# Performance work log

Hardware: AMD Instinct MI355X
Metric: run time of the kernel (lower is better)

The kernel has to match this reference:

```python
import jax, jax.numpy as jnp
import numpy as np

N, E, F_IN, HID, HEADS, NG, NC = 50000, 800000, 128, 64, 4, 64, 10
NEG_SLOPE = 0.2


def gat_conv(h_in, src, dst, W, att_src, att_dst, bias, heads, out_ch, concat, num_nodes):
    # h_in: [N, Fin]; W: [Fin, heads*out_ch]; att_*: [heads, out_ch]; bias: [heads*out_ch] or [out_ch]
    h = (h_in @ W).reshape(num_nodes, heads, out_ch)            # [N,H,C]
    a_src = jnp.sum(h * att_src, axis=-1)                        # [N,H]
    a_dst = jnp.sum(h * att_dst, axis=-1)                        # [N,H]
    alpha = jax.nn.leaky_relu(a_src[src] + a_dst[dst], NEG_SLOPE)  # [Etot,H]
    # softmax over incoming edges per destination node
    amax = jax.ops.segment_max(alpha, dst, num_segments=num_nodes)
    amax = jnp.where(jnp.isfinite(amax), amax, 0.0)
    ex = jnp.exp(alpha - amax[dst])
    denom = jax.ops.segment_sum(ex, dst, num_segments=num_nodes)
    w = ex / (denom[dst] + 1e-16)                                # [Etot,H]
    msg = h[src] * w[:, :, None]                                 # [Etot,H,C]
    out = jax.ops.segment_sum(msg, dst, num_segments=num_nodes)  # [N,H,C]
    out = out.reshape(num_nodes, heads * out_ch) if concat else out.mean(axis=1)
    return out + bias


def setup_inputs() -> dict:
    key = jax.random.key(0)
    ks = jax.random.split(key, 20)
    s = lambda k, shp, f: (jax.random.normal(k, shp, jnp.float32) * f)
    return {
        "x": jax.random.normal(ks[0], (N, F_IN), jnp.float32),
        "edge_index": jax.random.randint(ks[1], (2, E), 0, N, jnp.int32),
        "batch": jax.random.randint(ks[2], (N,), 0, NG, jnp.int32),
        "W_proj": s(ks[3], (F_IN, HID), 0.05), "b_proj": jnp.zeros((HID,), jnp.float32),
        "W1": s(ks[4], (HID, HEADS * HID), 0.05),
        "att_src1": s(ks[5], (HEADS, HID), 0.1), "att_dst1": s(ks[6], (HEADS, HID), 0.1),
        "b1": jnp.zeros((HEADS * HID,), jnp.float32),
        "W2": s(ks[7], (HEADS * HID, HID), 0.05),
        "att_src2": s(ks[8], (1, HID), 0.1), "att_dst2": s(ks[9], (1, HID), 0.1),
        "b2": jnp.zeros((HID,), jnp.float32),
        "W_fc1": s(ks[10], (HID, HID // 2), 0.05), "b_fc1": jnp.zeros((HID // 2,), jnp.float32),
        "W_fc2": s(ks[11], (HID // 2, NC), 0.05), "b_fc2": jnp.zeros((NC,), jnp.float32),
    }


def reference(x, edge_index, batch, W_proj, b_proj, W1, att_src1, att_dst1, b1,
              W2, att_src2, att_dst2, b2, W_fc1, b_fc1, W_fc2, b_fc2):
    n = x.shape[0]
    loops = jnp.arange(n, dtype=edge_index.dtype)  # PyG GATConv add_self_loops=True
    src = jnp.concatenate([edge_index[0], loops])
    dst = jnp.concatenate([edge_index[1], loops])
    h = jax.nn.relu(x @ W_proj + b_proj)                                  # feature_proj + relu
    h = gat_conv(h, src, dst, W1, att_src1, att_dst1, b1, HEADS, HID, True, n)
    h = jax.nn.leaky_relu(h, NEG_SLOPE)                                    # dropout = identity (eval)
    h = gat_conv(h, src, dst, W2, att_src2, att_dst2, b2, 1, HID, False, n)
    h = jax.nn.leaky_relu(h, NEG_SLOPE)
    cnt = jax.ops.segment_sum(jnp.ones((n,), h.dtype), batch, num_segments=NG)
    gmean = jax.ops.segment_sum(h, batch, num_segments=NG) / jnp.maximum(cnt, 1.0)[:, None]
    gmax = jax.ops.segment_max(h, batch, num_segments=NG)
    gmax = jnp.where(jnp.isfinite(gmax), gmax, 0.0)
    g = gmean + gmax
    g = jax.nn.relu(g @ W_fc1 + b_fc1)
    return jax.nn.log_softmax(g @ W_fc2 + b_fc2, axis=1)
```

## Files before the change

kernel.cpp:

```cpp
#include <hip/hip_runtime.h>
#include <math.h>

#define NN 50000
#define EE 800000
#define ET 850000
#define FIN 128
#define HD 64
#define NH 4
#define NGR 64
#define NCL 10
#define NEG 0.2f

typedef unsigned short u16;
typedef unsigned char u8;
typedef unsigned int u32;
typedef __attribute__((ext_vector_type(8))) short short8;
typedef __attribute__((ext_vector_type(4))) float f32x4;

__device__ __forceinline__ float lrelu(float x){ return x > 0.f ? x : NEG * x; }

__device__ __forceinline__ float wsum(float v){
#pragma unroll
  for (int o = 32; o > 0; o >>= 1) v += __shfl_xor(v, o, 64);
  return v;
}
__device__ __forceinline__ float wmax(float v){
#pragma unroll
  for (int o = 32; o > 0; o >>= 1) v = fmaxf(v, __shfl_xor(v, o, 64));
  return v;
}
__device__ __forceinline__ int esrc(const int* ei, int e){ return e < EE ? ei[e] : e - EE; }
__device__ __forceinline__ int edst(const int* ei, int e){ return e < EE ? ei[EE + e] : e - EE; }

__device__ __forceinline__ unsigned f2key(float f){
  unsigned u = __float_as_uint(f);
  return (u & 0x80000000u) ? ~u : (u | 0x80000000u);
}
__device__ __forceinline__ float key2f(unsigned k){
  return (k & 0x80000000u) ? __uint_as_float(k & 0x7fffffffu) : __uint_as_float(~k);
}

__device__ __forceinline__ u16 f2b(float f){
  u32 u = __float_as_uint(f);
  u32 r = (u + 0x7FFFu + ((u >> 16) & 1u)) >> 16;
  return (u16)r;
}
__device__ __forceinline__ float b2f(u16 b){ return __uint_as_float(((u32)b) << 16); }
__device__ __forceinline__ u32 pkbf16(float lo, float hi){
  u32 r;
  asm("v_cvt_pk_bf16_f32 %0, %1, %2" : "=v"(r) : "v"(lo), "v"(hi));
  return r;
}
__device__ __forceinline__ u8 f2fp8(float f){
  return (u8)__builtin_amdgcn_cvt_pk_fp8_f32(f, 0.f, 0, false);
}
__device__ __forceinline__ int rl(int v, int idx){ return __builtin_amdgcn_readlane(v, idx); }
__device__ __forceinline__ float rlf(float v, int idx){
  return __uint_as_float((u32)__builtin_amdgcn_readlane((int)__float_as_uint(v), idx));
}

__global__ __launch_bounds__(256) void k_phf(const int* __restrict__ ei, int* __restrict__ cnt,
            int* __restrict__ rank,
            const float* __restrict__ x, const float* __restrict__ Wp, const float* __restrict__ bp,
            const float* __restrict__ W1, const float* __restrict__ as1, const float* __restrict__ ad1,
            u8* __restrict__ h1f8, float* __restrict__ a_s, float* __restrict__ a_d, int gb){
  __shared__ u16 As[64*(FIN+8)];
  __shared__ u16 h0s[64*(HD+8)];
  int b = blockIdx.x;
  if (b >= gb){
    int base = (b - gb)*1024;
#pragma unroll
    for (int k = 0; k < 4; ++k){
      int e = base + k*256 + threadIdx.x;
      if (e < ET){
        int d = edst(ei, e);
        rank[e] = atomicAdd(&cnt[d], 1);
      }
    }
    return;
  }
  constexpr int LDK1 = FIN + 8;
  constexpr int LDH  = HD + 8;
  int t = threadIdx.x, w = t >> 6, l = t & 63;
  int l16 = l & 15, kg = l >> 4;

  short8 bfp[4];
#pragma unroll
  for (int kt = 0; kt < 4; ++kt){
    short8 v;
#pragma unroll
    for (int j = 0; j < 8; ++j) v[j] = (short)f2b(Wp[(size_t)(kt*32 + kg*8 + j)*HD + w*16 + l16]);
    bfp[kt] = v;
  }
  short8 bf1[2*4];
#pragma unroll
  for (int kt = 0; kt < 2; ++kt)
#pragma unroll
    for (int nt = 0; nt < 4; ++nt){
      short8 v;
#pragma unroll
      for (int j = 0; j < 8; ++j) v[j] = (short)f2b(W1[(size_t)(kt*32 + kg*8 + j)*256 + w*64 + nt*16 + l16]);
      bf1[kt*4 + nt] = v;
    }
  float bv = bp[w*16 + l16];
  float asv[4], adv[4];
#pragma unroll
  for (int nt = 0; nt < 4; ++nt){
    asv[nt] = as1[w*64 + nt*16 + l16];
    adv[nt] = ad1[w*64 + nt*16 + l16];
  }

  for (int ch = 0; ch < 2; ++ch){
    int nb = (b*2 + ch)*64;
    if (nb >= NN) break;
    __syncthreads();
    for (int u = t; u < 64*16; u += 256){
      int r = u >> 4, c = u & 15;
      int n = nb + r;
      uint4 v = make_uint4(0u,0u,0u,0u);
      if (n < NN){
        float4 f0 = *(const float4*)&x[(size_t)n*FIN + c*8];
        float4 f1 = *(const float4*)&x[(size_t)n*FIN + c*8 + 4];
        v = make_uint4(pkbf16(f0.x,f0.y), pkbf16(f0.z,f0.w), pkbf16(f1.x,f1.y), pkbf16(f1.z,f1.w));
      }
      *(uint4*)&As[r*LDK1 + c*8] = v;
    }
    __syncthreads();
#pragma unroll
    for (int rt = 0; rt < 4; ++rt){
      short8 afp[4];
#pragma unroll
      for (int kt = 0; kt < 4; ++kt)
        afp[kt] = *(const short8*)&As[(rt*16 + l16)*LDK1 + kt*32 + kg*8];
      f32x4 acc = (f32x4){0.f,0.f,0.f,0.f};
#pragma unroll
      for (int kt = 0; kt < 4; ++kt)
        acc = __builtin_amdgcn_mfma_f32_16x16x32_bf16(afp[kt], bfp[kt], acc, 0, 0, 0);
#pragma unroll
      for (int r4 = 0; r4 < 4; ++r4)
        h0s[(rt*16 + kg*4 + r4)*LDH + w*16 + l16] = f2b(fmaxf(acc[r4] + bv, 0.f));
    }
    __syncthreads();
#pragma unroll
    for (int rt = 0; rt < 4; ++rt){
      short8 af[2];
#pragma unroll
      for (int kt = 0; kt < 2; ++kt)
        af[kt] = *(const short8*)&h0s[(rt*16 + l16)*LDH + kt*32 + kg*8];
      f32x4 acc[4];
#pragma unroll
      for (int nt = 0; nt < 4; ++nt){
        acc[nt] = (f32x4){0.f,0.f,0.f,0.f};
#pragma unroll
        for (int kt = 0; kt < 2; ++kt)
          acc[nt] = __builtin_amdgcn_mfma_f32_16x16x32_bf16(af[kt], bf1[kt*4 + nt], acc[nt], 0, 0, 0);
      }
      int rbase = nb + rt*16 + kg*4;
#pragma unroll
      for (int nt = 0; nt < 4; ++nt)
#pragma unroll
        for (int r4 = 0; r4 < 4; ++r4){
          int n = rbase + r4;
          if (n < NN) h1f8[(size_t)n*256 + w*64 + nt*16 + l16] = f2fp8(acc[nt][r4]);
        }
#pragma unroll
      for (int r4 = 0; r4 < 4; ++r4){
        float ps = 0.f, pd = 0.f;
#pragma unroll
        for (int nt = 0; nt < 4; ++nt){
          ps = fmaf(acc[nt][r4], asv[nt], ps);
          pd = fmaf(acc[nt][r4], adv[nt], pd);
        }
#pragma unroll
        for (int o = 1; o < 16; o <<= 1){
          ps += __shfl_xor(ps, o, 64);
          pd += __shfl_xor(pd, o, 64);
        }
        int n = rbase + r4;
        if (l16 == 0 && n < NN){ a_s[n*NH + w] = ps; a_d[n*NH + w] = pd; }
      }
    }
  }
}

template<int K, int NOUT, int CPW>
__device__ __forceinline__ void gemm_body2(int bid, u16* As, float* sred,
            const u16* __restrict__ A, const float* __restrict__ Bf,
            const float* __restrict__ att_s, const float* __restrict__ att_d,
            u16* __restrict__ C, float* __restrict__ a_s, float* __restrict__ a_d){
  constexpr int KT = K/32;
  constexpr int NT = CPW/16;
  constexpr int LDK = K + 8;
  int t = threadIdx.x, w = t >> 6, l = t & 63;
  int c0 = w*CPW;
  int l16 = l & 15, kg = l >> 4;

  short8 bf[KT*NT];
#pragma unroll
  for (int kt = 0; kt < KT; ++kt)
#pragma unroll
    for (int nt = 0; nt < NT; ++nt){
      int kbase = kt*32 + kg*8;
      int col = c0 + nt*16 + l16;
      short8 v;
#pragma unroll
      for (int j = 0; j < 8; ++j) v[j] = (short)f2b(Bf[(size_t)(kbase + j)*NOUT + col]);
      bf[kt*NT + nt] = v;
    }
  float asv = att_s[c0 + l16], adv = att_d[c0 + l16];

  for (int ch = 0; ch < 2; ++ch){
    int nb = (bid*2 + ch)*64;
    if (nb >= NN) break;
    __syncthreads();
    constexpr int UPR = K/8;
    for (int u = t; u < 64*UPR; u += 256){
      int r = u / UPR, c = u % UPR;
      int n = nb + r;
      uint4 v = make_uint4(0u,0u,0u,0u);
      if (n < NN) v = *(const uint4*)&A[(size_t)n*K + c*8];
      *(uint4*)&As[r*LDK + c*8] = v;
    }
    __syncthreads();
#pragma unroll
    for (int rt = 0; rt < 4; ++rt){
      short8 af[KT];
#pragma unroll
      for (int kt = 0; kt < KT; ++kt)
        af[kt] = *(const short8*)&As[(rt*16 + l16)*LDK + kt*32 + kg*8];
      f32x4 acc = (f32x4){0.f,0.f,0.f,0.f};
#pragma unroll
      for (int kt = 0; kt < KT; ++kt)
        acc = __builtin_amdgcn_mfma_f32_16x16x32_bf16(af[kt], bf[kt], acc, 0, 0, 0);
      int rbase = nb + rt*16 + kg*4;
#pragma unroll
      for (int r4 = 0; r4 < 4; ++r4){
        int n = rbase + r4;
        if (n < NN) C[(size_t)n*NOUT + c0 + l16] = f2b(acc[r4]);
      }
#pragma unroll
      for (int r4 = 0; r4 < 4; ++r4){
        float ps = acc[r4]*asv;
        float pd = acc[r4]*adv;
#pragma unroll
        for (int o = 1; o < 16; o <<= 1){
          ps += __shfl_xor(ps, o, 64);
          pd += __shfl_xor(pd, o, 64);
        }
        if (l16 == 0){
          int row = rt*16 + kg*4 + r4;
          sred[(w*64 + row)*2]     = ps;
          sred[(w*64 + row)*2 + 1] = pd;
        }
      }
    }
    __syncthreads();
    if (t < 64){
      int n = nb + t;
      if (n < NN){
        float s = sred[t*2] + sred[(64+t)*2] + sred[(128+t)*2] + sred[(192+t)*2];
        float d = sred[t*2+1] + sred[(64+t)*2+1] + sred[(128+t)*2+1] + sred[(192+t)*2+1];
        a_s[n] = s; a_d[n] = d;
      }
    }
  }
}

__global__ void k_bsum(const int* __restrict__ cnt, int* __restrict__ bsums){
  int b = blockIdx.x, t = threadIdx.x;
  int i = b*256 + t;
  int v = (i < NN) ? cnt[i] : 0;
  float s = wsum((float)v);
  __shared__ float ws4[4];
  if ((t & 63) == 0) ws4[t >> 6] = s;
  __syncthreads();
  if (t == 0) bsums[b] = (int)(ws4[0] + ws4[1] + ws4[2] + ws4[3] + 0.5f);
}

__global__ __launch_bounds__(256) void k_off2(const int* __restrict__ cnt, const int* __restrict__ bsums,
                                              int* __restrict__ off){
  int b = blockIdx.x, t = threadIdx.x;
  int i = b*256 + t;
  __shared__ int s[256];
  __shared__ int w4[4];
  int v = (i < NN) ? cnt[i] : 0;
  s[t] = v; __syncthreads();
  for (int d = 1; d < 256; d <<= 1){
    int xv = (t >= d) ? s[t-d] : 0;
    __syncthreads();
    s[t] += xv;
    __syncthreads();
  }
  int pv = (t < b) ? bsums[t] : 0;
  int r = pv;
#pragma unroll
  for (int o2 = 32; o2 > 0; o2 >>= 1) r += __shfl_xor(r, o2, 64);
  if ((t & 63) == 0) w4[t >> 6] = r;
  __syncthreads();
  int pre = w4[0] + w4[1] + w4[2] + w4[3];
  if (i < NN) off[i] = pre + s[t] - v;
  if (i == NN - 1) off[NN] = pre + s[t];
}

__global__ __launch_bounds__(256) void k_scatter(const int* __restrict__ ei, const int* __restrict__ off,
            const int* __restrict__ rank, u16* __restrict__ csrc){
  int base = blockIdx.x*1024;
#pragma unroll
  for (int k = 0; k < 4; ++k){
    int e = base + k*256 + threadIdx.x;
    if (e < ET){
      int d = edst(ei, e);
      int s = esrc(ei, e);
      csrc[off[d] + rank[e]] = (u16)s;
    }
  }
}

__global__ __launch_bounds__(256) void k_feat2(const u16* __restrict__ h1outb, const float* __restrict__ W2,
            const float* __restrict__ as2, const float* __restrict__ ad2,
            u16* __restrict__ h2b, float* __restrict__ a_s, float* __restrict__ a_d){
  __shared__ u16 As[64*(256+8)];
  __shared__ float sred[4*64*2];
  gemm_body2<256, 64, 16>(blockIdx.x, As, sred, h1outb, W2, as2, ad2, h2b, a_s, a_d);
}

__global__ __launch_bounds__(256) void k_gat1(const u8* __restrict__ h1f8, const float* __restrict__ a_s,
                       const float* __restrict__ a_d, const int* __restrict__ off,
                       const u16* __restrict__ csrc, const float* __restrict__ b1,
                       u16* __restrict__ h1outb){
  __shared__ float lw[4][4][68];
  int wv = threadIdx.x >> 6, l = threadIdx.x & 63;
  int n = blockIdx.x*4 + wv;
  if (n >= NN) return;
  int e0 = off[n], e1 = off[n+1], deg = e1 - e0;
  int j16 = l & 15, h = l >> 4;
  float adst = a_d[n*NH + h];
  float acc0 = 0.f, acc1 = 0.f, acc2 = 0.f, acc3 = 0.f;
  const u8* base = h1f8 + 4*l;

#define GAT1_FMA8(wrd, wq) { \
  acc0 = fmaf(__builtin_amdgcn_cvt_f32_fp8((int)(wrd), 0), wq, acc0); \
  acc1 = fmaf(__builtin_amdgcn_cvt_f32_fp8((int)(wrd), 1), wq, acc1); \
  acc2 = fmaf(__builtin_amdgcn_cvt_f32_fp8((int)(wrd), 2), wq, acc2); \
  acc3 = fmaf(__builtin_amdgcn_cvt_f32_fp8((int)(wrd), 3), wq, acc3); }

  if (deg <= 64){
    int sreg[4]; float wreg[4];
#pragma unroll
    for (int c = 0; c < 4; ++c){
      int idx = c*16 + j16;
      int s = (idx < deg) ? (int)csrc[e0 + idx] : 0;
      sreg[c] = s;
      wreg[c] = (idx < deg) ? lrelu(a_s[s*NH + h] + adst) : -3.0e38f;
    }
    float m = fmaxf(fmaxf(wreg[0], wreg[1]), fmaxf(wreg[2], wreg[3]));
#pragma unroll
    for (int o2 = 1; o2 < 16; o2 <<= 1) m = fmaxf(m, __shfl_xor(m, o2, 64));
    float se = 0.f;
#pragma unroll
    for (int c = 0; c < 4; ++c){
      int idx = c*16 + j16;
      float wc = (idx < deg) ? __expf(wreg[c] - m) : 0.f;
      wreg[c] = wc; se += wc;
    }
#pragma unroll
    for (int o2 = 1; o2 < 16; o2 <<= 1) se += __shfl_xor(se, o2, 64);
    float inv = 1.f / (se + 1e-16f);
#pragma unroll
    for (int c = 0; c < 4; ++c) lw[wv][h][c*16 + j16] = wreg[c] * inv;

#pragma unroll
    for (int c = 0; c < 4; ++c){
      int cbase = c*16;
      if (cbase < deg){
        int cnt = deg - cbase; if (cnt > 16) cnt = 16;
        int j2 = 0;
        for (; j2 + 8 <= cnt; j2 += 8){
          float4 wqa = *(const float4*)&lw[wv][h][cbase + j2];
          float4 wqb = *(const float4*)&lw[wv][h][cbase + j2 + 4];
          int s0 = rl(sreg[c], j2),   s1 = rl(sreg[c], j2+1);
          int s2 = rl(sreg[c], j2+2), s3 = rl(sreg[c], j2+3);
          int s4 = rl(sreg[c], j2+4), s5 = rl(sreg[c], j2+5);
          int s6 = rl(sreg[c], j2+6), s7 = rl(sreg[c], j2+7);
          u32 w0 = *(const u32*)(base + (size_t)(u32)s0*256);
          u32 w1 = *(const u32*)(base + (size_t)(u32)s1*256);
          u32 w2 = *(const u32*)(base + (size_t)(u32)s2*256);
          u32 w3 = *(const u32*)(base + (size_t)(u32)s3*256);
          u32 w4 = *(const u32*)(base + (size_t)(u32)s4*256);
          u32 w5 = *(const u32*)(base + (size_t)(u32)s5*256);
          u32 w6 = *(const u32*)(base + (size_t)(u32)s6*256);
          u32 w7 = *(const u32*)(base + (size_t)(u32)s7*256);
          GAT1_FMA8(w0, wqa.x) GAT1_FMA8(w1, wqa.y) GAT1_FMA8(w2, wqa.z) GAT1_FMA8(w3, wqa.w)
          GAT1_FMA8(w4, wqb.x) GAT1_FMA8(w5, wqb.y) GAT1_FMA8(w6, wqb.z) GAT1_FMA8(w7, wqb.w)
        }
        for (; j2 + 4 <= cnt; j2 += 4){
          float4 wq = *(const float4*)&lw[wv][h][cbase + j2];
          int s0 = rl(sreg[c], j2),   s1 = rl(sreg[c], j2+1);
          int s2 = rl(sreg[c], j2+2), s3 = rl(sreg[c], j2+3);
          u32 w0 = *(const u32*)(base + (size_t)(u32)s0*256);
          u32 w1 = *(const u32*)(base + (size_t)(u32)s1*256);
          u32 w2 = *(const u32*)(base + (size_t)(u32)s2*256);
          u32 w3 = *(const u32*)(base + (size_t)(u32)s3*256);
          GAT1_FMA8(w0, wq.x) GAT1_FMA8(w1, wq.y) GAT1_FMA8(w2, wq.z) GAT1_FMA8(w3, wq.w)
        }
        for (; j2 < cnt; ++j2){
          float wqs = lw[wv][h][cbase + j2];
          int s = rl(sreg[c], j2);
          u32 wd = *(const u32*)(base + (size_t)(u32)s*256);
          GAT1_FMA8(wd, wqs)
        }
      }
    }
  } else {
    float m = -3.0e38f;
    for (int i = e0 + j16; i < e1; i += 16){
      int s = csrc[i];
      m = fmaxf(m, lrelu(a_s[s*NH + h] + adst));
    }
#pragma unroll
    for (int o2 = 1; o2 < 16; o2 <<= 1) m = fmaxf(m, __shfl_xor(m, o2, 64));
    float se = 0.f;
    for (int i = e0 + j16; i < e1; i += 16){
      int s = csrc[i];
      se += __expf(lrelu(a_s[s*NH + h] + adst) - m);
    }
#pragma unroll
    for (int o2 = 1; o2 < 16; o2 <<= 1) se += __shfl_xor(se, o2, 64);
    float inv = 1.f / (se + 1e-16f);
    for (int i = e0; i < e1; ++i){
      int s = csrc[i];
      float wq = __expf(lrelu(a_s[s*NH + h] + adst) - m) * inv;
      u32 wd = *(const u32*)(base + (size_t)(u32)s*256);
      GAT1_FMA8(wd, wq)
    }
  }
  float4 bv = *(const float4*)&b1[4*l];
  u32 lo = pkbf16(lrelu(acc0 + bv.x), lrelu(acc1 + bv.y));
  u32 hi = pkbf16(lrelu(acc2 + bv.z), lrelu(acc3 + bv.w));
  *(uint2*)&h1outb[(size_t)n*256 + 4*l] = make_uint2(lo, hi);
}

__global__ __launch_bounds__(256) void k_gat2(const u16* __restrict__ h2b, const float* __restrict__ a_s,
                       const float* __restrict__ a_d, const int* __restrict__ off,
                       const u16* __restrict__ csrc, const float* __restrict__ b2v,
                       float* __restrict__ h2out){
  int wv = threadIdx.x >> 6, l = threadIdx.x & 63;
  int n = blockIdx.x*4 + wv;
  if (n >= NN) return;
  int e0 = off[n], e1 = off[n+1], deg = e1 - e0;
  float adst = a_d[n];
  if (deg <= 64){
    int sA = 0; float alA = -3.0e38f;
    if (l < deg){
      sA = (int)csrc[e0 + l];
      alA = lrelu(a_s[sA] + adst);
    }
    float m = wmax(alA);
    float wA = (l < deg) ? __expf(alA - m) : 0.f;
    float se = wsum(wA);
    wA *= 1.f / (se + 1e-16f);
    float acc = 0.f;
    int idx = 0;
    for (; idx + 8 <= deg; idx += 8){
      int s0 = rl(sA, idx),   s1 = rl(sA, idx+1);
      int s2 = rl(sA, idx+2), s3 = rl(sA, idx+3);
      int s4 = rl(sA, idx+4), s5 = rl(sA, idx+5);
      int s6 = rl(sA, idx+6), s7 = rl(sA, idx+7);
      float w0 = rlf(wA, idx),   w1 = rlf(wA, idx+1);
      float w2 = rlf(wA, idx+2), w3 = rlf(wA, idx+3);
      float w4 = rlf(wA, idx+4), w5 = rlf(wA, idx+5);
      float w6 = rlf(wA, idx+6), w7 = rlf(wA, idx+7);
      float v0 = b2f(h2b[(size_t)(u32)s0*HD + l]);
      float v1 = b2f(h2b[(size_t)(u32)s1*HD + l]);
      float v2 = b2f(h2b[(size_t)(u32)s2*HD + l]);
      float v3 = b2f(h2b[(size_t)(u32)s3*HD + l]);
      float v4 = b2f(h2b[(size_t)(u32)s4*HD + l]);
      float v5 = b2f(h2b[(size_t)(u32)s5*HD + l]);
      float v6 = b2f(h2b[(size_t)(u32)s6*HD + l]);
      float v7 = b2f(h2b[(size_t)(u32)s7*HD + l]);
      acc = fmaf(v0, w0, acc); acc = fmaf(v1, w1, acc);
      acc = fmaf(v2, w2, acc); acc = fmaf(v3, w3, acc);
      acc = fmaf(v4, w4, acc); acc = fmaf(v5, w5, acc);
      acc = fmaf(v6, w6, acc); acc = fmaf(v7, w7, acc);
    }
    for (; idx < deg; ++idx){
      int s = rl(sA, idx);
      float w = rlf(wA, idx);
      acc = fmaf(b2f(h2b[(size_t)(u32)s*HD + l]), w, acc);
    }
    h2out[(size_t)n*HD + l] = lrelu(acc + b2v[l]);
  } else {
    float m = -3.0e38f;
    for (int i = e0 + l; i < e1; i += 64){
      int s = csrc[i];
      m = fmaxf(m, lrelu(a_s[s] + adst));
    }
    m = wmax(m);
    float se = 0.f;
    for (int i = e0 + l; i < e1; i += 64){
      int s = csrc[i];
      se += __expf(lrelu(a_s[s] + adst) - m);
    }
    se = wsum(se);
    float inv = 1.f / (se + 1e-16f);
    float acc = 0.f;
    for (int i = e0; i < e1; ++i){
      int s = csrc[i];
      acc += b2f(h2b[(size_t)s*HD + l]) * __expf(lrelu(a_s[s] + adst) - m);
    }
    h2out[(size_t)n*HD + l] = lrelu(acc*inv + b2v[l]);
  }
}


__global__ void k_pool(const float* __restrict__ h2out, const int* __restrict__ batch,
                       float* __restrict__ gsum, unsigned* __restrict__ gmaxk, int* __restrict__ gcnt){
  __shared__ float ssum[NGR*HD];
  __shared__ unsigned smax[NGR*HD];
  __shared__ int scnt[NGR];
  int t = threadIdx.x;
  for (int i = t; i < NGR*HD; i += 256){ ssum[i] = 0.f; smax[i] = 0u; }
  if (t < NGR) scnt[t] = 0;
  __syncthreads();
  int wv = t >> 6, lane = t & 63;
  for (int n = blockIdx.x*4 + wv; n < NN; n += gridDim.x*4){
    int g = batch[n];
    float v = h2out[(size_t)n*HD + lane];
    atomicAdd(&ssum[g*HD + lane], v);
    atomicMax(&smax[g*HD + lane], f2key(v));
    if (lane == 0) atomicAdd(&scnt[g], 1);
  }
  __syncthreads();
  for (int i = t; i < NGR*HD; i += 256){
    atomicAdd(&gsum[i], ssum[i]);
    atomicMax(&gmaxk[i], smax[i]);
  }
  if (t < NGR) atomicAdd(&gcnt[t], scnt[t]);
}


__global__ void k_final(const float* __restrict__ gsum, const unsigned* __restrict__ gmaxk,
                        const int* __restrict__ gcnt,
                        const float* __restrict__ Wf1, const float* __restrict__ bf1,
                        const float* __restrict__ Wf2, const float* __restrict__ bf2,
                        float* __restrict__ out){
  int g = blockIdx.x, t = threadIdx.x;
  __shared__ float gv[HD];
  __shared__ float f1[32];
  __shared__ float lg[NCL];
  int c = gcnt[g];
  float dn = fmaxf((float)c, 1.f);
  float mean = gsum[g*HD + t] / dn;
  float mx = (c > 0) ? key2f(gmaxk[g*HD + t]) : 0.f;
  gv[t] = mean + mx;
  __syncthreads();
  if (t < 32){
    float a = bf1[t];
#pragma unroll
    for (int k = 0; k < HD; ++k) a += gv[k] * Wf1[k*32 + t];
    f1[t] = a > 0.f ? a : 0.f;
  }
  __syncthreads();
  if (t < NCL){
    float a = bf2[t];
#pragma unroll
    for (int k = 0; k < 32; ++k) a += f1[k] * Wf2[k*NCL + t];
    lg[t] = a;
  }
  __syncthreads();
  if (t < NCL){
    float m = lg[0];
#pragma unroll
    for (int i = 1; i < NCL; ++i) m = fmaxf(m, lg[i]);
    float s = 0.f;
#pragma unroll
    for (int i = 0; i < NCL; ++i) s += expf(lg[i] - m);
    out[g*NCL + t] = lg[t] - m - logf(s);
  }
}

extern "C" void kernel_launch(void* const* d_in, const int* in_sizes, int n_in,
                              void* d_out, int out_size, void* d_ws, size_t ws_size,
                              hipStream_t stream) {
  const float* x   = (const float*)d_in[0];
  const int*   ei  = (const int*)d_in[1];
  const int*   bat = (const int*)d_in[2];
  const float* Wp  = (const float*)d_in[3];
  const float* bp  = (const float*)d_in[4];
  const float* W1  = (const float*)d_in[5];
  const float* as1 = (const float*)d_in[6];
  const float* ad1 = (const float*)d_in[7];
  const float* b1  = (const float*)d_in[8];
  const float* W2  = (const float*)d_in[9];
  const float* as2 = (const float*)d_in[10];
  const float* ad2 = (const float*)d_in[11];
  const float* b2  = (const float*)d_in[12];
  const float* Wf1 = (const float*)d_in[13];
  const float* bf1 = (const float*)d_in[14];
  const float* Wf2 = (const float*)d_in[15];
  const float* bf2 = (const float*)d_in[16];
  float* out = (float*)d_out;

  char* base = (char*)d_ws;
  size_t o = 0;
  auto alloc = [&](size_t elems) -> char* {
    char* p = base + o*4;
    o += (elems + 63) & ~(size_t)63;
    return p;
  };
  u8*    h1f8   = (u8*)alloc(3200000);
  u16*   h1outb = (u16*)alloc(6400000);
  u16*   h2b    = (u16*)alloc(1600000);
  float* h2out  = (float*)alloc(3200000);
  float* a_s1   = (float*)alloc(200000);
  float* a_d1   = (float*)alloc(200000);
  float* a_s2   = (float*)alloc(50000);
  float* a_d2   = (float*)alloc(50000);
  int*   off    = (int*)alloc(50001);
  int*   rank   = (int*)alloc(850000);
  int*   bsums  = (int*)alloc(256);
  u16*   csrc   = (u16*)alloc(425000);
  int*   cnt    = (int*)alloc(50000);
  float* gsum   = (float*)alloc(NGR*HD);
  unsigned* gmaxk = (unsigned*)alloc(NGR*HD);
  int*   gcnt   = (int*)alloc(NGR);

  const int NB  = (NN + 255) / 256;
  const int EB4 = (ET + 1023) / 1024;
  const int GB  = (NN + 127) / 128;
  const int WB  = (NN + 3) / 4;

  hipMemsetAsync(cnt, 0, NN*sizeof(int), stream);
  hipMemsetAsync(gsum, 0, (NGR*HD*2 + 64)*sizeof(int), stream);

  k_phf<<<GB + EB4, 256, 0, stream>>>(ei, cnt, rank, x, Wp, bp, W1, as1, ad1, h1f8, a_s1, a_d1, GB);
  k_bsum<<<NB, 256, 0, stream>>>(cnt, bsums);
  k_off2<<<NB, 256, 0, stream>>>(cnt, bsums, off);
  k_scatter<<<EB4, 256, 0, stream>>>(ei, off, rank, csrc);

  k_gat1<<<WB, 256, 0, stream>>>(h1f8, a_s1, a_d1, off, csrc, b1, h1outb);

  k_feat2<<<GB, 256, 0, stream>>>(h1outb, W2, as2, ad2, h2b, a_s2, a_d2);
  k_gat2<<<WB, 256, 0, stream>>>(h2b, a_s2, a_d2, off, csrc, b2, h2out);

  k_pool<<<256, 256, 0, stream>>>(h2out, bat, gsum, gmaxk, gcnt);

  k_final<<<NGR, 64, 0, stream>>>(gsum, gmaxk, gcnt, Wf1, bf1, Wf2, bf2, out);
}
```

Baseline: 201.3 us.

## Build CSR via two-level bucketed radix partition instead of global atomics

Replaces the per-edge global atomic counting plus rank/scatter pipeline with a two-pass bucket partition. Edges are first grouped into 256-node buckets using per-block LDS histograms and a scan. Each bucket's edges are then finished inside a block of the fused projection kernel, using LDS atomics to produce the offsets and the sorted source list. This is meant to cut global atomic contention and make the scatter writes more local. The cost is extra kernels, more scans and a packed intermediate buffer. It also simplifies gemm_body2's B-fragment load to a single N tile.

```diff
diff --git a/kernel.cpp b/kernel.cpp
--- a/kernel.cpp
+++ b/kernel.cpp
@@ -10,6 +10,8 @@
 #define NGR 64
 #define NCL 10
 #define NEG 0.2f
+#define NBK 196
+#define ECH 831
 
 typedef unsigned short u16;
 typedef unsigned char u8;
@@ -29,6 +31,11 @@
   for (int o = 32; o > 0; o >>= 1) v = fmaxf(v, __shfl_xor(v, o, 64));
   return v;
 }
+__device__ __forceinline__ int wsumi(int v){
+#pragma unroll
+  for (int o = 32; o > 0; o >>= 1) v += __shfl_xor(v, o, 64);
+  return v;
+}
 __device__ __forceinline__ int esrc(const int* ei, int e){ return e < EE ? ei[e] : e - EE; }
 __device__ __forceinline__ int edst(const int* ei, int e){ return e < EE ? ei[EE + e] : e - EE; }
 
@@ -59,29 +66,127 @@
   return __uint_as_float((u32)__builtin_amdgcn_readlane((int)__float_as_uint(v), idx));
 }
 
-__global__ __launch_bounds__(256) void k_phf(const int* __restrict__ ei, int* __restrict__ cnt,
-            int* __restrict__ rank,
+__global__ __launch_bounds__(256) void k_b1hist(const int* __restrict__ ei, int* __restrict__ bcnt){
+  __shared__ int lc[NBK];
+  int t = threadIdx.x, blk = blockIdx.x;
+  for (int i = t; i < NBK; i += 256) lc[i] = 0;
+  __syncthreads();
+#pragma unroll
+  for (int k = 0; k < 4; ++k){
+    int e = blk*1024 + k*256 + t;
+    if (e < ET) atomicAdd(&lc[edst(ei, e) >> 8], 1);
+  }
+  __syncthreads();
+  for (int i = t; i < NBK; i += 256) bcnt[i*ECH + blk] = lc[i];
+}
+
+__global__ __launch_bounds__(256) void k_bscana(const int* __restrict__ bcnt, int* __restrict__ btot){
+  int b = blockIdx.x, t = threadIdx.x;
+  int s = 0;
+  for (int j = t; j < ECH; j += 256) s += bcnt[b*ECH + j];
+  s = wsumi(s);
+  __shared__ int w4[4];
+  if ((t & 63) == 0) w4[t >> 6] = s;
+  __syncthreads();
+  if (t == 0) btot[b] = w4[0] + w4[1] + w4[2] + w4[3];
+}
+
+__global__ __launch_bounds__(256) void k_bscanb(const int* __restrict__ bcnt, const int* __restrict__ btot,
+                                                int* __restrict__ boff, int* __restrict__ bb){
+  int b = blockIdx.x, t = threadIdx.x;
+  int pv = (t < b) ? btot[t] : 0;
+  int r = wsumi(pv);
+  __shared__ int w4[4];
+  if ((t & 63) == 0) w4[t >> 6] = r;
+  __syncthreads();
+  int base = w4[0] + w4[1] + w4[2] + w4[3];
+  if (t == 0) bb[b] = base;
+  __shared__ int s[256];
+  int carry = 0;
+  for (int j0 = 0; j0 < ECH; j0 += 256){
+    int j = j0 + t;
+    int v = (j < ECH) ? bcnt[b*ECH + j] : 0;
+    s[t] = v; __syncthreads();
+    for (int d = 1; d < 256; d <<= 1){
+      int xv = (t >= d) ? s[t-d] : 0;
+      __syncthreads();
+      s[t] += xv;
+      __syncthreads();
+    }
+    int excl = s[t] - v;
+    if (j < ECH) boff[b*ECH + j] = base + carry + excl;
+    int tot = s[255];
+    __syncthreads();
+    carry += tot;
+  }
+}
+
+__global__ __launch_bounds__(256) void k_b1scat(const int* __restrict__ ei, const int* __restrict__ boff,
+                                                u32* __restrict__ packed){
+  __shared__ int lpos[NBK];
+  int t = threadIdx.x, blk = blockIdx.x;
+  for (int i = t; i < NBK; i += 256) lpos[i] = boff[i*ECH + blk];
+  __syncthreads();
+#pragma unroll
+  for (int k = 0; k < 4; ++k){
+    int e = blk*1024 + k*256 + t;
+    if (e < ET){
+      int d = edst(ei, e);
+      int s = esrc(ei, e);
+      int slot = atomicAdd(&lpos[d >> 8], 1);
+      packed[slot] = ((u32)(d & 255) << 16) | (u32)s;
+    }
+  }
+}
+
+__global__ __launch_bounds__(256) void k_phf2(
+            const u32* __restrict__ packed, const int* __restrict__ btot, const int* __restrict__ bb,
+            int* __restrict__ off, u16* __restrict__ csrc,
             const float* __restrict__ x, const float* __restrict__ Wp, const float* __restrict__ bp,
             const float* __restrict__ W1, const float* __restrict__ as1, const float* __restrict__ ad1,
             u8* __restrict__ h1f8, float* __restrict__ a_s, float* __restrict__ a_d, int gb){
   __shared__ u16 As[64*(FIN+8)];
   __shared__ u16 h0s[64*(HD+8)];
-  int b = blockIdx.x;
-  if (b >= gb){
-    int base = (b - gb)*1024;
-#pragma unroll
-    for (int k = 0; k < 4; ++k){
-      int e = base + k*256 + threadIdx.x;
-      if (e < ET){
-        int d = edst(ei, e);
-        rank[e] = atomicAdd(&cnt[d], 1);
-      }
+  __shared__ int hc[256];
+  __shared__ int sc[256];
+  __shared__ int pp[256];
+  int t = threadIdx.x;
+  int bid = blockIdx.x;
+  if (bid >= gb){
+    int b = bid - gb;
+    int e0 = bb[b];
+    int cntb = btot[b];
+    hc[t] = 0;
+    __syncthreads();
+    for (int i = t; i < cntb; i += 256){
+      u32 p = packed[e0 + i];
+      atomicAdd(&hc[p >> 16], 1);
+    }
+    __syncthreads();
+    int v = hc[t];
+    sc[t] = v; __syncthreads();
+    for (int d = 1; d < 256; d <<= 1){
+      int xv = (t >= d) ? sc[t-d] : 0;
+      __syncthreads();
+      sc[t] += xv;
+      __syncthreads();
+    }
+    int excl = sc[t] - v;
+    int node = b*256 + t;
+    if (node < NN) off[node] = e0 + excl;
+    if (b == 0 && t == 0) off[NN] = ET;
+    pp[t] = excl;
+    __syncthreads();
+    for (int i = t; i < cntb; i += 256){
+      u32 p = packed[e0 + i];
+      int slot = atomicAdd(&pp[p >> 16], 1);
+      csrc[(size_t)e0 + slot] = (u16)(p & 0xFFFFu);
     }
     return;
   }
   constexpr int LDK1 = FIN + 8;
   constexpr int LDH  = HD + 8;
-  int t = threadIdx.x, w = t >> 6, l = t & 63;
+  int w = t >> 6, l = t & 63;
   int l16 = l & 15, kg = l >> 4;
 
   short8 bfp[4];
@@ -111,7 +216,7 @@
   }
 
   for (int ch = 0; ch < 2; ++ch){
-    int nb = (b*2 + ch)*64;
+    int nb = (bid*2 + ch)*64;
     if (nb >= NN) break;
     __syncthreads();
     for (int u = t; u < 64*16; u += 256){
@@ -189,24 +294,21 @@
             const float* __restrict__ att_s, const float* __restrict__ att_d,
             u16* __restrict__ C, float* __restrict__ a_s, float* __restrict__ a_d){
   constexpr int KT = K/32;
-  constexpr int NT = CPW/16;
   constexpr int LDK = K + 8;
   int t = threadIdx.x, w = t >> 6, l = t & 63;
   int c0 = w*CPW;
   int l16 = l & 15, kg = l >> 4;
 
-  short8 bf[KT*NT];
-#pragma unroll
-  for (int kt = 0; kt < KT; ++kt)
-#pragma unroll
-    for (int nt = 0; nt < NT; ++nt){
-      int kbase = kt*32 + kg*8;
-      int col = c0 + nt*16 + l16;
-      short8 v;
-#pragma unroll
-      for (int j = 0; j < 8; ++j) v[j] = (short)f2b(Bf[(size_t)(kbase + j)*NOUT + col]);
-      bf[kt*NT + nt] = v;
-    }
+  short8 bf[KT];
+#pragma unroll
+  for (int kt = 0; kt < KT; ++kt){
+    int kbase = kt*32 + kg*8;
+    int col = c0 + l16;
+    short8 v;
+#pragma unroll
+    for (int j = 0; j < 8; ++j) v[j] = (short)f2b(Bf[(size_t)(kbase + j)*NOUT + col]);
+    bf[kt] = v;
+  }
   float asv = att_s[c0 + l16], adv = att_d[c0 + l16];
 
   for (int ch = 0; ch < 2; ++ch){
@@ -262,56 +364,6 @@
         float d = sred[t*2+1] + sred[(64+t)*2+1] + sred[(128+t)*2+1] + sred[(192+t)*2+1];
         a_s[n] = s; a_d[n] = d;
       }
-    }
-  }
-}
-
-__global__ void k_bsum(const int* __restrict__ cnt, int* __restrict__ bsums){
-  int b = blockIdx.x, t = threadIdx.x;
-  int i = b*256 + t;
-  int v = (i < NN) ? cnt[i] : 0;
-  float s = wsum((float)v);
-  __shared__ float ws4[4];
-  if ((t & 63) == 0) ws4[t >> 6] = s;
-  __syncthreads();
-  if (t == 0) bsums[b] = (int)(ws4[0] + ws4[1] + ws4[2] + ws4[3] + 0.5f);
-}
-
-__global__ __launch_bounds__(256) void k_off2(const int* __restrict__ cnt, const int* __restrict__ bsums,
-                                              int* __restrict__ off){
-  int b = blockIdx.x, t = threadIdx.x;
-  int i = b*256 + t;
-  __shared__ int s[256];
-  __shared__ int w4[4];
-  int v = (i < NN) ? cnt[i] : 0;
-  s[t] = v; __syncthreads();
-  for (int d = 1; d < 256; d <<= 1){
-    int xv = (t >= d) ? s[t-d] : 0;
-    __syncthreads();
-    s[t] += xv;
-    __syncthreads();
-  }
-  int pv = (t < b) ? bsums[t] : 0;
-  int r = pv;
-#pragma unroll
-  for (int o2 = 32; o2 > 0; o2 >>= 1) r += __shfl_xor(r, o2, 64);
-  if ((t & 63) == 0) w4[t >> 6] = r;
-  __syncthreads();
-  int pre = w4[0] + w4[1] + w4[2] + w4[3];
-  if (i < NN) off[i] = pre + s[t] - v;
-  if (i == NN - 1) off[NN] = pre + s[t];
-}
-
-__global__ __launch_bounds__(256) void k_scatter(const int* __restrict__ ei, const int* __restrict__ off,
-            const int* __restrict__ rank, u16* __restrict__ csrc){
-  int base = blockIdx.x*1024;
-#pragma unroll
-  for (int k = 0; k < 4; ++k){
-    int e = base + k*256 + threadIdx.x;
-    if (e < ET){
-      int d = edst(ei, e);
-      int s = esrc(ei, e);
-      csrc[off[d] + rank[e]] = (u16)s;
     }
   }
 }
@@ -617,26 +669,28 @@
   float* a_s2   = (float*)alloc(50000);
   float* a_d2   = (float*)alloc(50000);
   int*   off    = (int*)alloc(50001);
-  int*   rank   = (int*)alloc(850000);
-  int*   bsums  = (int*)alloc(256);
+  int*   bcnt   = (int*)alloc(NBK*ECH);
+  int*   boff   = (int*)alloc(NBK*ECH);
+  int*   btot   = (int*)alloc(256);
+  int*   bb     = (int*)alloc(256);
+  u32*   packed = (u32*)alloc(850000);
   u16*   csrc   = (u16*)alloc(425000);
-  int*   cnt    = (int*)alloc(50000);
   float* gsum   = (float*)alloc(NGR*HD);
   unsigned* gmaxk = (unsigned*)alloc(NGR*HD);
   int*   gcnt   = (int*)alloc(NGR);
 
-  const int NB  = (NN + 255) / 256;
-  const int EB4 = (ET + 1023) / 1024;
   const int GB  = (NN + 127) / 128;
   const int WB  = (NN + 3) / 4;
 
-  hipMemsetAsync(cnt, 0, NN*sizeof(int), stream);
   hipMemsetAsync(gsum, 0, (NGR*HD*2 + 64)*sizeof(int), stream);
 
-  k_phf<<<GB + EB4, 256, 0, stream>>>(ei, cnt, rank, x, Wp, bp, W1, as1, ad1, h1f8, a_s1, a_d1, GB);
-  k_bsum<<<NB, 256, 0, stream>>>(cnt, bsums);
-  k_off2<<<NB, 256, 0, stream>>>(cnt, bsums, off);
-  k_scatter<<<EB4, 256, 0, stream>>>(ei, off, rank, csrc);
+  k_b1hist<<<ECH, 256, 0, stream>>>(ei, bcnt);
+  k_bscana<<<NBK, 256, 0, stream>>>(bcnt, btot);
+  k_bscanb<<<NBK, 256, 0, stream>>>(bcnt, btot, boff, bb);
+  k_b1scat<<<ECH, 256, 0, stream>>>(ei, boff, packed);
+
+  k_phf2<<<GB + NBK, 256, 0, stream>>>(packed, btot, bb, off, csrc,
+                                       x, Wp, bp, W1, as1, ad1, h1f8, a_s1, a_d1, GB);
 
   k_gat1<<<WB, 256, 0, stream>>>(h1f8, a_s1, a_d1, off, csrc, b1, h1outb);
 
```

New measurement: 175.9 us. 12.7% less time.
